# Performance work log

Measured on AMD Instinct MI355X. Metric: run time of the kernel, lower is better.

## Reference

```python
import jax, jax.numpy as jnp
import numpy as np

D_MODEL = 1024
NUM_HEADS = 16
D_K = D_MODEL // NUM_HEADS
B, S = 2, 2048


def setup_inputs() -> dict:
    key = jax.random.key(0)
    ks = jax.random.split(key, 12)
    sc = 1.0 / np.sqrt(D_MODEL)
    inp = {
        'q': jax.random.normal(ks[0], (B, S, D_MODEL), jnp.float32),
        'k': jax.random.normal(ks[1], (B, S, D_MODEL), jnp.float32),
        'v': jax.random.normal(ks[2], (B, S, D_MODEL), jnp.float32),
        'mask': jnp.tril(jnp.ones((S, S), jnp.int32))[None, None, :, :],  # causal, 1=keep
        'wq': jax.random.normal(ks[3], (D_MODEL, D_MODEL), jnp.float32) * sc,
        'bq': jnp.zeros((D_MODEL,), jnp.float32),
        'wk': jax.random.normal(ks[4], (D_MODEL, D_MODEL), jnp.float32) * sc,
        'bk': jnp.zeros((D_MODEL,), jnp.float32),
        'wv': jax.random.normal(ks[5], (D_MODEL, D_MODEL), jnp.float32) * sc,
        'bv': jnp.zeros((D_MODEL,), jnp.float32),
        'wo': jax.random.normal(ks[6], (D_MODEL, D_MODEL), jnp.float32) * sc,
        'bo': jnp.zeros((D_MODEL,), jnp.float32),
    }
    return inp


def _split_heads(x):
    b, s, _ = x.shape
    return x.reshape(b, s, NUM_HEADS, D_K).transpose(0, 2, 1, 3)  # (B,H,S,Dk)


def reference(q, k, v, mask, wq, bq, wk, bk, wv, bv, wo, bo):
    qh = _split_heads(q @ wq + bq)
    kh = _split_heads(k @ wk + bk)
    vh = _split_heads(v @ wv + bv)
    scores = jnp.einsum('bhqd,bhkd->bhqk', qh, kh) / jnp.sqrt(jnp.float32(D_K))
    scores = jnp.where(mask == 0, jnp.float32(-1e9), scores)
    attn = jax.nn.softmax(scores, axis=-1)  # dropout is identity in eval
    ctx = jnp.einsum('bhqk,bhkd->bhqd', attn, vh)
    ctx = ctx.transpose(0, 2, 1, 3).reshape(q.shape[0], q.shape[1], D_MODEL)
    out = ctx @ wo + bo
    return out, attn
```

## Files before the change

kernel.cpp:

```cpp
#include <hip/hip_runtime.h>


#define D_MODEL 1024
#define NH      16
#define DK      64
#define BATCH   2
#define SEQ     2048
#define MTOT    (BATCH * SEQ)

typedef __attribute__((ext_vector_type(8))) short bf16x8;
typedef __attribute__((ext_vector_type(4))) float f32x4;

__device__ __forceinline__ unsigned short f2bf(float f) {
    unsigned u = __float_as_uint(f);
    u += 0x7fff + ((u >> 16) & 1);
    return (unsigned short)(u >> 16);
}

__device__ __forceinline__ void async_ld16(void* lds, const void* g) {
    __builtin_amdgcn_global_load_lds(
        (const __attribute__((address_space(1))) void*)g,
        (__attribute__((address_space(3))) void*)lds, 16, 0, 0);
}

__global__ __launch_bounds__(256)
void cast_f32_bf16(const float* __restrict__ src, unsigned short* __restrict__ dst, int n4)
{
    int i = blockIdx.x * 256 + threadIdx.x;
    if (i < n4) {
        float4 v = ((const float4*)src)[i];
        uint2 w;
        w.x = (unsigned)f2bf(v.x) | ((unsigned)f2bf(v.y) << 16);
        w.y = (unsigned)f2bf(v.z) | ((unsigned)f2bf(v.w) << 16);
        ((uint2*)dst)[i] = w;
    }
}

__global__ __launch_bounds__(256)
void transpose_cast_w(const float* __restrict__ w0, const float* __restrict__ w1,
                      const float* __restrict__ w2, const float* __restrict__ w3,
                      unsigned short* __restrict__ dst)
{
    const float* W = blockIdx.z == 0 ? w0 : blockIdx.z == 1 ? w1 : blockIdx.z == 2 ? w2 : w3;
    unsigned short* Wt = dst + (size_t)blockIdx.z * (D_MODEL * D_MODEL);
    __shared__ float t[32][33];
    const int tx = threadIdx.x & 31, ty = threadIdx.x >> 5;
    const int k0 = blockIdx.x * 32, n0 = blockIdx.y * 32;
#pragma unroll
    for (int r = 0; r < 4; ++r)
        t[ty + r * 8][tx] = W[(size_t)(k0 + ty + r * 8) * D_MODEL + n0 + tx];
    __syncthreads();
#pragma unroll
    for (int r = 0; r < 4; ++r)
        Wt[(size_t)(n0 + ty + r * 8) * D_MODEL + k0 + tx] = f2bf(t[tx][ty + r * 8]);
}

__global__ __launch_bounds__(256)
void gemm_mfma(const unsigned short* __restrict__ A0, const unsigned short* __restrict__ A1,
               const unsigned short* __restrict__ A2, const unsigned short* __restrict__ WT,
               const float* __restrict__ b0, const float* __restrict__ b1,
               const float* __restrict__ b2,
               unsigned short* __restrict__ D0, unsigned short* __restrict__ D1,
               unsigned short* __restrict__ D2, float* __restrict__ Dout, int mode)
{
    const int K = D_MODEL;
    __shared__ unsigned short As[128 * 32];
    __shared__ unsigned short Bs[128 * 32];

    const int z = blockIdx.z;
    const unsigned short* A = (mode == 0) ? (z == 0 ? A0 : z == 1 ? A1 : A2) : A0;
    const unsigned short* Wt = (mode == 0) ? WT + (size_t)z * (D_MODEL * D_MODEL) : WT;
    const float* bias = (z == 0 ? b0 : z == 1 ? b1 : b2);

    const int tid = threadIdx.x;
    const int wave = tid >> 6, lane = tid & 63;
    const int quad = lane >> 4, l15 = lane & 15;
    const int m0 = blockIdx.x * 128, n0 = blockIdx.y * 128;
    const int wm = (wave & 1) * 64, wn = (wave >> 1) * 64;

    const int srow = (lane >> 2);
    const int skel = (lane & 3) * 8;
    const unsigned short* gA0 = A  + (size_t)(m0 + wave * 32 +      srow) * K + skel;
    const unsigned short* gA1 = A  + (size_t)(m0 + wave * 32 + 16 + srow) * K + skel;
    const unsigned short* gB0 = Wt + (size_t)(n0 + wave * 32 +      srow) * K + skel;
    const unsigned short* gB1 = Wt + (size_t)(n0 + wave * 32 + 16 + srow) * K + skel;
    unsigned short* lA0 = &As[(wave * 2 + 0) * 512];
    unsigned short* lA1 = &As[(wave * 2 + 1) * 512];
    unsigned short* lB0 = &Bs[(wave * 2 + 0) * 512];
    unsigned short* lB1 = &Bs[(wave * 2 + 1) * 512];

    f32x4 acc[4][4];
#pragma unroll
    for (int i = 0; i < 4; ++i)
#pragma unroll
        for (int j = 0; j < 4; ++j) acc[i][j] = (f32x4){0.f, 0.f, 0.f, 0.f};

    for (int k0 = 0; k0 < K; k0 += 32) {
        __syncthreads();
        async_ld16(lA0, gA0 + k0);
        async_ld16(lA1, gA1 + k0);
        async_ld16(lB0, gB0 + k0);
        async_ld16(lB1, gB1 + k0);
        __syncthreads();
        bf16x8 a[4], b[4];
#pragma unroll
        for (int i = 0; i < 4; ++i)
            a[i] = *(const bf16x8*)&As[(wm + i * 16 + l15) * 32 + quad * 8];
#pragma unroll
        for (int j = 0; j < 4; ++j)
            b[j] = *(const bf16x8*)&Bs[(wn + j * 16 + l15) * 32 + quad * 8];
#pragma unroll
        for (int i = 0; i < 4; ++i)
#pragma unroll
            for (int j = 0; j < 4; ++j)
                acc[i][j] = __builtin_amdgcn_mfma_f32_16x16x32_bf16(a[i], b[j], acc[i][j], 0, 0, 0);
    }

    unsigned short* Dh = (z == 0 ? D0 : z == 1 ? D1 : D2);
#pragma unroll
    for (int j = 0; j < 4; ++j) {
        const int col = n0 + wn + j * 16 + l15;
        const float bv = bias[col];
        const int h = col >> 6, d = col & 63;
#pragma unroll
        for (int i = 0; i < 4; ++i) {
            const int row0 = m0 + wm + i * 16 + quad * 4;
            if (mode == 0 && z == 2) {
                const int bb = row0 >> 11, ss = row0 & (SEQ - 1);
                uint2 w2;
                w2.x = (unsigned)f2bf(acc[i][j][0] + bv) | ((unsigned)f2bf(acc[i][j][1] + bv) << 16);
                w2.y = (unsigned)f2bf(acc[i][j][2] + bv) | ((unsigned)f2bf(acc[i][j][3] + bv) << 16);
                *(uint2*)&Dh[(((size_t)bb * NH + h) * DK + d) * SEQ + ss] = w2;
            } else {
#pragma unroll
                for (int r = 0; r < 4; ++r) {
                    const int row = row0 + r;
                    const float val = acc[i][j][r] + bv;
                    if (mode == 0) {
                        const int bb = row >> 11, ss = row & (SEQ - 1);
                        Dh[(((size_t)bb * NH + h) * SEQ + ss) * DK + d] = f2bf(val);
                    } else {
                        Dout[(size_t)row * D_MODEL + col] = val;
                    }
                }
            }
        }
    }
}

__global__ __launch_bounds__(256)
void attn_fused(const unsigned short* __restrict__ Qp, const unsigned short* __restrict__ Kp,
                const unsigned short* __restrict__ Vtp, float* __restrict__ attn,
                unsigned short* __restrict__ ctxb)
{
    __shared__ unsigned short Ks[64 * 64];
    __shared__ unsigned short Vs[64 * 64];
    __shared__ unsigned short Pb[64 * 72];

    const int tid  = threadIdx.x;
    const int w    = tid >> 6;
    const int lane = tid & 63;
    const int l15  = lane & 15;
    const int hi   = lane >> 4;
    const int qt   = blockIdx.x;
    const int bh   = blockIdx.y;
    const int q0   = qt * 64;

    const unsigned short* Qh = Qp  + (size_t)bh * SEQ * DK;
    const unsigned short* Kh = Kp  + (size_t)bh * SEQ * DK;
    const unsigned short* Vh = Vtp + (size_t)bh * DK * SEQ;
    float* attn_h = attn + (size_t)bh * SEQ * SEQ;
    const int bb = bh >> 4, hh = bh & 15;
    unsigned short* ctx_h = ctxb + (size_t)bb * SEQ * D_MODEL + hh * DK;

    const int srow = w * 16 + (lane >> 3);
    const int sswz = (lane & 7) ^ (srow & 7);
    const unsigned short* gK0 = Kh + (size_t)srow * DK + sswz * 8;
    const unsigned short* gK1 = Kh + (size_t)(srow + 8) * DK + sswz * 8;
    const unsigned short* gV0 = Vh + (size_t)srow * SEQ + sswz * 8;
    const unsigned short* gV1 = Vh + (size_t)(srow + 8) * SEQ + sswz * 8;
    unsigned short* lK0 = &Ks[w * 1024];
    unsigned short* lK1 = &Ks[w * 1024 + 512];
    unsigned short* lV0 = &Vs[w * 1024];
    unsigned short* lV1 = &Vs[w * 1024 + 512];

    const int qrow = q0 + w * 16 + l15;
    const bf16x8 qf0 = *(const bf16x8*)(Qh + (size_t)qrow * DK + hi * 8);
    const bf16x8 qf1 = *(const bf16x8*)(Qh + (size_t)qrow * DK + 32 + hi * 8);

    const int swz = (l15 & 7) << 4;

    float run_m = -1e30f, run_l = 0.f;
    for (int kt = 0; kt <= qt; ++kt) {
        __syncthreads();
        async_ld16(lK0, gK0 + (size_t)kt * 64 * DK);
        async_ld16(lK1, gK1 + (size_t)kt * 64 * DK);
        __syncthreads();
        f32x4 s[4];
#pragma unroll
        for (int kk = 0; kk < 4; ++kk) {
            const char* kb = (const char*)Ks + (kk * 16 + l15) * 128;
            bf16x8 k0 = *(const bf16x8*)(kb + ((hi * 16) ^ swz));
            bf16x8 k1 = *(const bf16x8*)(kb + ((64 + hi * 16) ^ swz));
            f32x4 z = (f32x4){0.f, 0.f, 0.f, 0.f};
            z = __builtin_amdgcn_mfma_f32_16x16x32_bf16(k0, qf0, z, 0, 0, 0);
            s[kk] = __builtin_amdgcn_mfma_f32_16x16x32_bf16(k1, qf1, z, 0, 0, 0);
        }
        float tm = -1e30f;
#pragma unroll
        for (int kk = 0; kk < 4; ++kk)
#pragma unroll
            for (int r = 0; r < 4; ++r) {
                const int key = kt * 64 + kk * 16 + hi * 4 + r;
                const float x = (key <= qrow) ? s[kk][r] * 0.125f : -1e30f;
                s[kk][r] = x;
                tm = fmaxf(tm, x);
            }
        tm = fmaxf(tm, __shfl_xor(tm, 16));
        tm = fmaxf(tm, __shfl_xor(tm, 32));
        const float nm = fmaxf(run_m, tm);
        float sum = 0.f;
#pragma unroll
        for (int kk = 0; kk < 4; ++kk)
#pragma unroll
            for (int r = 0; r < 4; ++r)
                sum += __expf(s[kk][r] - nm);
        sum += __shfl_xor(sum, 16);
        sum += __shfl_xor(sum, 32);
        run_l = run_l * __expf(run_m - nm) + sum;
        run_m = nm;
    }
    const float m_f = run_m;
    const float linv = 1.f / run_l;

    f32x4 acc_pv[4];
#pragma unroll
    for (int jt = 0; jt < 4; ++jt) acc_pv[jt] = (f32x4){0.f, 0.f, 0.f, 0.f};

    for (int kt = 0; kt <= qt; ++kt) {
        __syncthreads();
        async_ld16(lK0, gK0 + (size_t)kt * 64 * DK);
        async_ld16(lK1, gK1 + (size_t)kt * 64 * DK);
        async_ld16(lV0, gV0 + kt * 64);
        async_ld16(lV1, gV1 + kt * 64);
        __syncthreads();
        f32x4 s[4];
#pragma unroll
        for (int kk = 0; kk < 4; ++kk) {
            const char* kb = (const char*)Ks + (kk * 16 + l15) * 128;
            bf16x8 k0 = *(const bf16x8*)(kb + ((hi * 16) ^ swz));
            bf16x8 k1 = *(const bf16x8*)(kb + ((64 + hi * 16) ^ swz));
            f32x4 z = (f32x4){0.f, 0.f, 0.f, 0.f};
            z = __builtin_amdgcn_mfma_f32_16x16x32_bf16(k0, qf0, z, 0, 0, 0);
            s[kk] = __builtin_amdgcn_mfma_f32_16x16x32_bf16(k1, qf1, z, 0, 0, 0);
        }
#pragma unroll
        for (int kk = 0; kk < 4; ++kk) {
            float p[4];
#pragma unroll
            for (int r = 0; r < 4; ++r) {
                const int key = kt * 64 + kk * 16 + hi * 4 + r;
                p[r] = (key <= qrow) ? __expf(s[kk][r] * 0.125f - m_f) * linv : 0.f;
            }
            float4 pv;
            pv.x = p[0]; pv.y = p[1]; pv.z = p[2]; pv.w = p[3];
            *(float4*)&attn_h[(size_t)qrow * SEQ + kt * 64 + kk * 16 + hi * 4] = pv;
            uint2 w2;
            w2.x = (unsigned)f2bf(p[0]) | ((unsigned)f2bf(p[1]) << 16);
            w2.y = (unsigned)f2bf(p[2]) | ((unsigned)f2bf(p[3]) << 16);
            *(uint2*)((char*)Pb + (size_t)(w * 16 + l15) * 144 + kk * 32 + hi * 8) = w2;
        }
        __syncthreads();
        const char* pbase = (const char*)Pb + (size_t)(w * 16 + l15) * 144;
        bf16x8 pa0 = *(const bf16x8*)(pbase + (hi * 16));
        bf16x8 pa1 = *(const bf16x8*)(pbase + (64 + hi * 16));
#pragma unroll
        for (int jt = 0; jt < 4; ++jt) {
            const char* vb = (const char*)Vs + (jt * 16 + l15) * 128;
            bf16x8 v0 = *(const bf16x8*)(vb + ((hi * 16) ^ swz));
            bf16x8 v1 = *(const bf16x8*)(vb + ((64 + hi * 16) ^ swz));
            acc_pv[jt] = __builtin_amdgcn_mfma_f32_16x16x32_bf16(pa0, v0, acc_pv[jt], 0, 0, 0);
            acc_pv[jt] = __builtin_amdgcn_mfma_f32_16x16x32_bf16(pa1, v1, acc_pv[jt], 0, 0, 0);
        }
    }

    const float4 zf = make_float4(0.f, 0.f, 0.f, 0.f);
    for (int kt = qt + 1; kt < SEQ / 64; ++kt) {
#pragma unroll
        for (int kk = 0; kk < 4; ++kk)
            *(float4*)&attn_h[(size_t)qrow * SEQ + kt * 64 + kk * 16 + hi * 4] = zf;
    }

#pragma unroll
    for (int jt = 0; jt < 4; ++jt) {
        const int d = jt * 16 + l15;
#pragma unroll
        for (int r = 0; r < 4; ++r) {
            const int qq = q0 + w * 16 + hi * 4 + r;
            ctx_h[(size_t)qq * D_MODEL + d] = f2bf(acc_pv[jt][r]);
        }
    }
}

extern "C" void kernel_launch(void* const* d_in, const int* in_sizes, int n_in,
                              void* d_out, int out_size, void* d_ws, size_t ws_size,
                              hipStream_t stream)
{
    const float* q  = (const float*)d_in[0];
    const float* k  = (const float*)d_in[1];
    const float* v  = (const float*)d_in[2];
    const float* wq = (const float*)d_in[4];
    const float* bq = (const float*)d_in[5];
    const float* wk = (const float*)d_in[6];
    const float* bk = (const float*)d_in[7];
    const float* wv = (const float*)d_in[8];
    const float* bv = (const float*)d_in[9];
    const float* wo = (const float*)d_in[10];
    const float* bo = (const float*)d_in[11];

    float* out  = (float*)d_out;
    float* attn = out + (size_t)BATCH * SEQ * D_MODEL;

    const size_t NE = (size_t)MTOT * D_MODEL;
    const size_t WE = (size_t)D_MODEL * D_MODEL;
    unsigned short* ws  = (unsigned short*)d_ws;
    unsigned short* qb  = ws;
    unsigned short* kb  = qb + NE;
    unsigned short* vb  = kb + NE;
    unsigned short* wT  = vb + NE;
    unsigned short* Qp  = wT + 4 * WE;
    unsigned short* Kp  = Qp + NE;
    unsigned short* Vt  = Kp + NE;
    unsigned short* ctxb = Vt + NE;

    const int n4 = (int)(NE / 4);
    cast_f32_bf16<<<(n4 + 255) / 256, 256, 0, stream>>>(q, qb, n4);
    cast_f32_bf16<<<(n4 + 255) / 256, 256, 0, stream>>>(k, kb, n4);
    cast_f32_bf16<<<(n4 + 255) / 256, 256, 0, stream>>>(v, vb, n4);
    transpose_cast_w<<<dim3(32, 32, 4), 256, 0, stream>>>(wq, wk, wv, wo, wT);

    gemm_mfma<<<dim3(32, 8, 3), 256, 0, stream>>>(qb, kb, vb, wT, bq, bk, bv,
                                                  Qp, Kp, Vt, nullptr, 0);

    dim3 ga(SEQ / 64, BATCH * NH);
    attn_fused<<<ga, 256, 0, stream>>>(Qp, Kp, Vt, attn, ctxb);

    gemm_mfma<<<dim3(32, 8, 1), 256, 0, stream>>>(ctxb, nullptr, nullptr, wT + 3 * WE,
                                                  bo, nullptr, nullptr,
                                                  nullptr, nullptr, nullptr, out, 1);
}
```

Before: 835.5 us.

## Double-buffer LDS tiles in GEMM and attention, shuffle P in registers, merge casts

Gives the GEMM and both attention passes double-buffered LDS tiles, so the async global-to-LDS load of the next tile overlaps the MFMA work on the current one and each iteration needs one barrier instead of two. The GEMM LDS layout gets an XOR swizzle to cut bank conflicts. In attention, the bf16 probability fragment is redistributed with cross-lane shuffles instead of a round trip through the shared P buffer and its barrier. The three input cast launches are merged into one. LDS use doubles and the many shuffles cost some VALU time; the output is dominated by the fp32 attention-matrix write, which this does not reduce.

After: 820.3 us. Within noise of the previous version (-1.8%).

```diff
diff --git a/kernel.cpp b/kernel.cpp
--- a/kernel.cpp
+++ b/kernel.cpp
@@ -16,6 +16,9 @@
     u += 0x7fff + ((u >> 16) & 1);
     return (unsigned short)(u >> 16);
 }
+__device__ __forceinline__ unsigned pk2(float a, float b) {
+    return (unsigned)f2bf(a) | ((unsigned)f2bf(b) << 16);
+}
 
 __device__ __forceinline__ void async_ld16(void* lds, const void* g) {
     __builtin_amdgcn_global_load_lds(
@@ -24,15 +27,18 @@
 }
 
 __global__ __launch_bounds__(256)
-void cast_f32_bf16(const float* __restrict__ src, unsigned short* __restrict__ dst, int n4)
-{
+void cast3_f32_bf16(const float* __restrict__ q, const float* __restrict__ k,
+                    const float* __restrict__ v, unsigned short* __restrict__ dst, int n4)
+{
+    const float* src = blockIdx.y == 0 ? q : blockIdx.y == 1 ? k : v;
+    unsigned short* d = dst + (size_t)blockIdx.y * ((size_t)n4 * 4);
     int i = blockIdx.x * 256 + threadIdx.x;
     if (i < n4) {
-        float4 v = ((const float4*)src)[i];
+        float4 t = ((const float4*)src)[i];
         uint2 w;
-        w.x = (unsigned)f2bf(v.x) | ((unsigned)f2bf(v.y) << 16);
-        w.y = (unsigned)f2bf(v.z) | ((unsigned)f2bf(v.w) << 16);
-        ((uint2*)dst)[i] = w;
+        w.x = pk2(t.x, t.y);
+        w.y = pk2(t.z, t.w);
+        ((uint2*)d)[i] = w;
     }
 }
 
@@ -64,8 +70,8 @@
                unsigned short* __restrict__ D2, float* __restrict__ Dout, int mode)
 {
     const int K = D_MODEL;
-    __shared__ unsigned short As[128 * 32];
-    __shared__ unsigned short Bs[128 * 32];
+    __shared__ unsigned short As[2][128 * 32];
+    __shared__ unsigned short Bs[2][128 * 32];
 
     const int z = blockIdx.z;
     const unsigned short* A = (mode == 0) ? (z == 0 ? A0 : z == 1 ? A1 : A2) : A0;
@@ -79,15 +85,11 @@
     const int wm = (wave & 1) * 64, wn = (wave >> 1) * 64;
 
     const int srow = (lane >> 2);
-    const int skel = (lane & 3) * 8;
+    const int skel = (((lane & 3) ^ ((srow >> 1) & 3)) * 8);
     const unsigned short* gA0 = A  + (size_t)(m0 + wave * 32 +      srow) * K + skel;
     const unsigned short* gA1 = A  + (size_t)(m0 + wave * 32 + 16 + srow) * K + skel;
     const unsigned short* gB0 = Wt + (size_t)(n0 + wave * 32 +      srow) * K + skel;
     const unsigned short* gB1 = Wt + (size_t)(n0 + wave * 32 + 16 + srow) * K + skel;
-    unsigned short* lA0 = &As[(wave * 2 + 0) * 512];
-    unsigned short* lA1 = &As[(wave * 2 + 1) * 512];
-    unsigned short* lB0 = &Bs[(wave * 2 + 0) * 512];
-    unsigned short* lB1 = &Bs[(wave * 2 + 1) * 512];
 
     f32x4 acc[4][4];
 #pragma unroll
@@ -95,25 +97,34 @@
 #pragma unroll
         for (int j = 0; j < 4; ++j) acc[i][j] = (f32x4){0.f, 0.f, 0.f, 0.f};
 
+    auto stage = [&](int buf, int k0) {
+        async_ld16(&As[buf][(wave * 2 + 0) * 512], gA0 + k0);
+        async_ld16(&As[buf][(wave * 2 + 1) * 512], gA1 + k0);
+        async_ld16(&Bs[buf][(wave * 2 + 0) * 512], gB0 + k0);
+        async_ld16(&Bs[buf][(wave * 2 + 1) * 512], gB1 + k0);
+    };
+
+    stage(0, 0);
+    __syncthreads();
+    int cur = 0;
+    const int rsw = (l15 >> 1) & 3;
+
     for (int k0 = 0; k0 < K; k0 += 32) {
-        __syncthreads();
-        async_ld16(lA0, gA0 + k0);
-        async_ld16(lA1, gA1 + k0);
-        async_ld16(lB0, gB0 + k0);
-        async_ld16(lB1, gB1 + k0);
-        __syncthreads();
+        if (k0 + 32 < K) stage(cur ^ 1, k0 + 32);
         bf16x8 a[4], b[4];
 #pragma unroll
         for (int i = 0; i < 4; ++i)
-            a[i] = *(const bf16x8*)&As[(wm + i * 16 + l15) * 32 + quad * 8];
+            a[i] = *(const bf16x8*)&As[cur][(wm + i * 16 + l15) * 32 + ((quad ^ rsw) << 3)];
 #pragma unroll
         for (int j = 0; j < 4; ++j)
-            b[j] = *(const bf16x8*)&Bs[(wn + j * 16 + l15) * 32 + quad * 8];
+            b[j] = *(const bf16x8*)&Bs[cur][(wn + j * 16 + l15) * 32 + ((quad ^ rsw) << 3)];
 #pragma unroll
         for (int i = 0; i < 4; ++i)
 #pragma unroll
             for (int j = 0; j < 4; ++j)
                 acc[i][j] = __builtin_amdgcn_mfma_f32_16x16x32_bf16(a[i], b[j], acc[i][j], 0, 0, 0);
+        __syncthreads();
+        cur ^= 1;
     }
 
     unsigned short* Dh = (z == 0 ? D0 : z == 1 ? D1 : D2);
@@ -128,8 +139,8 @@
             if (mode == 0 && z == 2) {
                 const int bb = row0 >> 11, ss = row0 & (SEQ - 1);
                 uint2 w2;
-                w2.x = (unsigned)f2bf(acc[i][j][0] + bv) | ((unsigned)f2bf(acc[i][j][1] + bv) << 16);
-                w2.y = (unsigned)f2bf(acc[i][j][2] + bv) | ((unsigned)f2bf(acc[i][j][3] + bv) << 16);
+                w2.x = pk2(acc[i][j][0] + bv, acc[i][j][1] + bv);
+                w2.y = pk2(acc[i][j][2] + bv, acc[i][j][3] + bv);
                 *(uint2*)&Dh[(((size_t)bb * NH + h) * DK + d) * SEQ + ss] = w2;
             } else {
 #pragma unroll
@@ -153,9 +164,8 @@
                 const unsigned short* __restrict__ Vtp, float* __restrict__ attn,
                 unsigned short* __restrict__ ctxb)
 {
-    __shared__ unsigned short Ks[64 * 64];
-    __shared__ unsigned short Vs[64 * 64];
-    __shared__ unsigned short Pb[64 * 72];
+    __shared__ unsigned short Ks[2][64 * 64];
+    __shared__ unsigned short Vs[2][64 * 64];
 
     const int tid  = threadIdx.x;
     const int w    = tid >> 6;
@@ -179,10 +189,15 @@
     const unsigned short* gK1 = Kh + (size_t)(srow + 8) * DK + sswz * 8;
     const unsigned short* gV0 = Vh + (size_t)srow * SEQ + sswz * 8;
     const unsigned short* gV1 = Vh + (size_t)(srow + 8) * SEQ + sswz * 8;
-    unsigned short* lK0 = &Ks[w * 1024];
-    unsigned short* lK1 = &Ks[w * 1024 + 512];
-    unsigned short* lV0 = &Vs[w * 1024];
-    unsigned short* lV1 = &Vs[w * 1024 + 512];
+
+    auto stageK = [&](int buf, int kt) {
+        async_ld16(&Ks[buf][w * 1024],       gK0 + (size_t)kt * 64 * DK);
+        async_ld16(&Ks[buf][w * 1024 + 512], gK1 + (size_t)kt * 64 * DK);
+    };
+    auto stageV = [&](int buf, int kt) {
+        async_ld16(&Vs[buf][w * 1024],       gV0 + kt * 64);
+        async_ld16(&Vs[buf][w * 1024 + 512], gV1 + kt * 64);
+    };
 
     const int qrow = q0 + w * 16 + l15;
     const bf16x8 qf0 = *(const bf16x8*)(Qh + (size_t)qrow * DK + hi * 8);
@@ -191,20 +206,20 @@
     const int swz = (l15 & 7) << 4;
 
     float run_m = -1e30f, run_l = 0.f;
+    stageK(0, 0);
+    __syncthreads();
+    int cur = 0;
     for (int kt = 0; kt <= qt; ++kt) {
-        __syncthreads();
-        async_ld16(lK0, gK0 + (size_t)kt * 64 * DK);
-        async_ld16(lK1, gK1 + (size_t)kt * 64 * DK);
-        __syncthreads();
+        if (kt < qt) stageK(cur ^ 1, kt + 1);
         f32x4 s[4];
 #pragma unroll
         for (int kk = 0; kk < 4; ++kk) {
-            const char* kb = (const char*)Ks + (kk * 16 + l15) * 128;
+            const char* kb = (const char*)&Ks[cur][0] + (kk * 16 + l15) * 128;
             bf16x8 k0 = *(const bf16x8*)(kb + ((hi * 16) ^ swz));
             bf16x8 k1 = *(const bf16x8*)(kb + ((64 + hi * 16) ^ swz));
-            f32x4 z = (f32x4){0.f, 0.f, 0.f, 0.f};
-            z = __builtin_amdgcn_mfma_f32_16x16x32_bf16(k0, qf0, z, 0, 0, 0);
-            s[kk] = __builtin_amdgcn_mfma_f32_16x16x32_bf16(k1, qf1, z, 0, 0, 0);
+            f32x4 zz = (f32x4){0.f, 0.f, 0.f, 0.f};
+            zz = __builtin_amdgcn_mfma_f32_16x16x32_bf16(k0, qf0, zz, 0, 0, 0);
+            s[kk] = __builtin_amdgcn_mfma_f32_16x16x32_bf16(k1, qf1, zz, 0, 0, 0);
         }
         float tm = -1e30f;
 #pragma unroll
@@ -229,6 +244,8 @@
         sum += __shfl_xor(sum, 32);
         run_l = run_l * __expf(run_m - nm) + sum;
         run_m = nm;
+        __syncthreads();
+        cur ^= 1;
     }
     const float m_f = run_m;
     const float linv = 1.f / run_l;
@@ -237,51 +254,67 @@
 #pragma unroll
     for (int jt = 0; jt < 4; ++jt) acc_pv[jt] = (f32x4){0.f, 0.f, 0.f, 0.f};
 
+    stageK(0, 0);
+    stageV(0, 0);
+    __syncthreads();
+    cur = 0;
+    const int srcA = l15 + 32 * (hi & 1);
+    const int srcB = srcA + 16;
+    const bool hiSel = (hi >> 1) != 0;
+
     for (int kt = 0; kt <= qt; ++kt) {
-        __syncthreads();
-        async_ld16(lK0, gK0 + (size_t)kt * 64 * DK);
-        async_ld16(lK1, gK1 + (size_t)kt * 64 * DK);
-        async_ld16(lV0, gV0 + kt * 64);
-        async_ld16(lV1, gV1 + kt * 64);
-        __syncthreads();
+        if (kt < qt) { stageK(cur ^ 1, kt + 1); stageV(cur ^ 1, kt + 1); }
         f32x4 s[4];
 #pragma unroll
         for (int kk = 0; kk < 4; ++kk) {
-            const char* kb = (const char*)Ks + (kk * 16 + l15) * 128;
+            const char* kb = (const char*)&Ks[cur][0] + (kk * 16 + l15) * 128;
             bf16x8 k0 = *(const bf16x8*)(kb + ((hi * 16) ^ swz));
             bf16x8 k1 = *(const bf16x8*)(kb + ((64 + hi * 16) ^ swz));
-            f32x4 z = (f32x4){0.f, 0.f, 0.f, 0.f};
-            z = __builtin_amdgcn_mfma_f32_16x16x32_bf16(k0, qf0, z, 0, 0, 0);
-            s[kk] = __builtin_amdgcn_mfma_f32_16x16x32_bf16(k1, qf1, z, 0, 0, 0);
-        }
+            f32x4 zz = (f32x4){0.f, 0.f, 0.f, 0.f};
+            zz = __builtin_amdgcn_mfma_f32_16x16x32_bf16(k0, qf0, zz, 0, 0, 0);
+            s[kk] = __builtin_amdgcn_mfma_f32_16x16x32_bf16(k1, qf1, zz, 0, 0, 0);
+        }
+        float pv[4][4];
 #pragma unroll
         for (int kk = 0; kk < 4; ++kk) {
-            float p[4];
 #pragma unroll
             for (int r = 0; r < 4; ++r) {
                 const int key = kt * 64 + kk * 16 + hi * 4 + r;
-                p[r] = (key <= qrow) ? __expf(s[kk][r] * 0.125f - m_f) * linv : 0.f;
+                pv[kk][r] = (key <= qrow) ? __expf(s[kk][r] * 0.125f - m_f) * linv : 0.f;
             }
-            float4 pv;
-            pv.x = p[0]; pv.y = p[1]; pv.z = p[2]; pv.w = p[3];
-            *(float4*)&attn_h[(size_t)qrow * SEQ + kt * 64 + kk * 16 + hi * 4] = pv;
-            uint2 w2;
-            w2.x = (unsigned)f2bf(p[0]) | ((unsigned)f2bf(p[1]) << 16);
-            w2.y = (unsigned)f2bf(p[2]) | ((unsigned)f2bf(p[3]) << 16);
-            *(uint2*)((char*)Pb + (size_t)(w * 16 + l15) * 144 + kk * 32 + hi * 8) = w2;
-        }
-        __syncthreads();
-        const char* pbase = (const char*)Pb + (size_t)(w * 16 + l15) * 144;
-        bf16x8 pa0 = *(const bf16x8*)(pbase + (hi * 16));
-        bf16x8 pa1 = *(const bf16x8*)(pbase + (64 + hi * 16));
+            float4 st;
+            st.x = pv[kk][0]; st.y = pv[kk][1]; st.z = pv[kk][2]; st.w = pv[kk][3];
+            *(float4*)&attn_h[(size_t)qrow * SEQ + kt * 64 + kk * 16 + hi * 4] = st;
+        }
+        unsigned D00 = pk2(pv[0][0], pv[0][1]), D01 = pk2(pv[0][2], pv[0][3]);
+        unsigned D10 = pk2(pv[1][0], pv[1][1]), D11 = pk2(pv[1][2], pv[1][3]);
+        unsigned D20 = pk2(pv[2][0], pv[2][1]), D21 = pk2(pv[2][2], pv[2][3]);
+        unsigned D30 = pk2(pv[3][0], pv[3][1]), D31 = pk2(pv[3][2], pv[3][3]);
+        unsigned a00 = __shfl((int)D00, srcA), a10 = __shfl((int)D10, srcA);
+        unsigned a01 = __shfl((int)D01, srcA), a11 = __shfl((int)D11, srcA);
+        unsigned b00 = __shfl((int)D00, srcB), b10 = __shfl((int)D10, srcB);
+        unsigned b01 = __shfl((int)D01, srcB), b11 = __shfl((int)D11, srcB);
+        unsigned a20 = __shfl((int)D20, srcA), a30 = __shfl((int)D30, srcA);
+        unsigned a21 = __shfl((int)D21, srcA), a31 = __shfl((int)D31, srcA);
+        unsigned b20 = __shfl((int)D20, srcB), b30 = __shfl((int)D30, srcB);
+        unsigned b21 = __shfl((int)D21, srcB), b31 = __shfl((int)D31, srcB);
+        uint4 u0, u1;
+        u0.x = hiSel ? a10 : a00;  u0.y = hiSel ? a11 : a01;
+        u0.z = hiSel ? b10 : b00;  u0.w = hiSel ? b11 : b01;
+        u1.x = hiSel ? a30 : a20;  u1.y = hiSel ? a31 : a21;
+        u1.z = hiSel ? b30 : b20;  u1.w = hiSel ? b31 : b21;
+        bf16x8 pa0 = *(bf16x8*)&u0;
+        bf16x8 pa1 = *(bf16x8*)&u1;
 #pragma unroll
         for (int jt = 0; jt < 4; ++jt) {
-            const char* vb = (const char*)Vs + (jt * 16 + l15) * 128;
+            const char* vb = (const char*)&Vs[cur][0] + (jt * 16 + l15) * 128;
             bf16x8 v0 = *(const bf16x8*)(vb + ((hi * 16) ^ swz));
             bf16x8 v1 = *(const bf16x8*)(vb + ((64 + hi * 16) ^ swz));
             acc_pv[jt] = __builtin_amdgcn_mfma_f32_16x16x32_bf16(pa0, v0, acc_pv[jt], 0, 0, 0);
             acc_pv[jt] = __builtin_amdgcn_mfma_f32_16x16x32_bf16(pa1, v1, acc_pv[jt], 0, 0, 0);
         }
+        __syncthreads();
+        cur ^= 1;
     }
 
     const float4 zf = make_float4(0.f, 0.f, 0.f, 0.f);
@@ -334,9 +367,7 @@
     unsigned short* ctxb = Vt + NE;
 
     const int n4 = (int)(NE / 4);
-    cast_f32_bf16<<<(n4 + 255) / 256, 256, 0, stream>>>(q, qb, n4);
-    cast_f32_bf16<<<(n4 + 255) / 256, 256, 0, stream>>>(k, kb, n4);
-    cast_f32_bf16<<<(n4 + 255) / 256, 256, 0, stream>>>(v, vb, n4);
+    cast3_f32_bf16<<<dim3((n4 + 255) / 256, 3), 256, 0, stream>>>(q, k, v, qb, n4);
     transpose_cast_w<<<dim3(32, 32, 4), 256, 0, stream>>>(wq, wk, wv, wo, wT);
 
     gemm_mfma<<<dim3(32, 8, 3), 256, 0, stream>>>(qb, kb, vb, wT, bq, bk, bv,
```
